# Performance work log

Measured on AMD Instinct MI355X. Metric: run time of the kernel, lower is better.

The kernel has to match this reference:

```python
import jax, jax.numpy as jnp
import numpy as np

NUM_NODES = 100000
NUM_EDGES = 1600000
EMBED_DIM = 128
NUM_CLASSES = 2
NUM_LAYERS = 3


def setup_inputs() -> dict:
    key = jax.random.key(0)
    k_row, k_col, k_val, k_emb, k_a, k_w, k_b = jax.random.split(key, 7)
    node_indices = jnp.arange(NUM_NODES, dtype=jnp.int64 if jax.config.read('jax_enable_x64') else jnp.int32)
    adj_row = jax.random.randint(k_row, (NUM_EDGES,), 0, NUM_NODES)
    adj_col = jax.random.randint(k_col, (NUM_EDGES,), 0, NUM_NODES)
    # symmetric-normalized-ish positive edge weights
    adj_val = jax.random.uniform(k_val, (NUM_EDGES,), dtype=jnp.float32) * (1.0 / 16.0)
    embedding = jax.random.normal(k_emb, (NUM_NODES, EMBED_DIM), dtype=jnp.float32)
    alpha = jnp.ones((NUM_LAYERS + 1,), dtype=jnp.float32) / (NUM_LAYERS + 1)
    W = jax.random.normal(k_w, (EMBED_DIM, NUM_CLASSES), dtype=jnp.float32) * 0.05
    b = jnp.zeros((NUM_CLASSES,), dtype=jnp.float32)
    return {
        'node_indices': node_indices, 'adj_row': adj_row, 'adj_col': adj_col,
        'adj_val': adj_val, 'embedding': embedding, 'alpha': alpha, 'W': W, 'b': b,
    }


def reference(node_indices, adj_row, adj_col, adj_val, embedding, alpha, W, b):
    # x: [N, D] embedding lookup
    x = embedding[node_indices]
    a = jax.nn.softmax(alpha)
    # alpha-weighted running sum over propagation layers (dropout in eval mode = identity)
    acc = a[0] * x
    cur = x
    for i in range(NUM_LAYERS):
        # sparse SpMM: out[r] += val * cur[c] for each edge (r, c)
        msgs = adj_val[:, None] * cur[adj_col]          # [E, D]
        cur = jax.ops.segment_sum(msgs, adj_row, num_segments=NUM_NODES)
        acc = acc + a[i + 1] * cur
    return acc @ W + b  # [N, num_classes]
```

## Files before the change

### kernel.cpp

```cpp
#include <hip/hip_runtime.h>

#define GD(x,y) (((x)+(y)-1)/(y))

#define SH    10
#define BPR   (1 << SH)
#define BS    256
#define KSPL  24
#define CAPSH 15
#define CAP   (1 << CAPSH)
#define CHUNK 2048

static __device__ __forceinline__ float2 ntload2(const float2* p){
    unsigned long long u = __builtin_nontemporal_load((const unsigned long long*)p);
    return *(float2*)&u;
}
static __device__ __forceinline__ void ntstore2(float2* p, float2 v){
    __builtin_nontemporal_store(*(unsigned long long*)&v, (unsigned long long*)p);
}

__global__ void init_k(int* __restrict__ cursor, int NBK,
                       const float* __restrict__ alpha, float* __restrict__ a, int na){
    int t = threadIdx.x;
    if (t < NBK) cursor[t] = t << CAPSH;
    if (t == 0){
        float m = alpha[0];
        for (int i = 1; i < na; ++i) m = fmaxf(m, alpha[i]);
        float s = 0.f;
        for (int i = 0; i < na; ++i){ float e = expf(alpha[i] - m); a[i] = e; s += e; }
        float inv = 1.f / s;
        for (int i = 0; i < na; ++i) a[i] *= inv;
    }
}

__global__ void fillproj_k(const int* __restrict__ row, const int* __restrict__ col,
                           const float* __restrict__ val, int* __restrict__ cursor,
                           int2* __restrict__ sep, int E, int NBK, int GF,
                           const float* __restrict__ emb, const int* __restrict__ idx,
                           const float* __restrict__ W, const float* __restrict__ bb,
                           const float* __restrict__ a, float* __restrict__ y,
                           float* __restrict__ out, int N){
    if (blockIdx.x < GF){
        __shared__ int2 staged[CHUNK];
        __shared__ unsigned char bid[CHUNK];
        __shared__ int h[128], sc[128], lstart[128], gbase[128], lcur[128];
        int t = threadIdx.x;
        int s = blockIdx.x * CHUNK;
        int e = min(E, s + CHUNK);
        int cnt = e - s;
        if (t < 128) h[t] = 0;
        __syncthreads();
        for (int base = s + t * 4; base < e; base += BS * 4){
            if (base + 3 < e){
                int4 r4 = *(const int4*)(row + base);
                atomicAdd(&h[r4.x >> SH], 1);
                atomicAdd(&h[r4.y >> SH], 1);
                atomicAdd(&h[r4.z >> SH], 1);
                atomicAdd(&h[r4.w >> SH], 1);
            } else {
                for (int j = 0; j < 4 && base + j < e; ++j)
                    atomicAdd(&h[row[base + j] >> SH], 1);
            }
        }
        __syncthreads();
        int v = (t < 128) ? h[t] : 0;
        if (t < 128) sc[t] = v;
        __syncthreads();
        #pragma unroll
        for (int off = 1; off < 128; off <<= 1){
            int add = (t < 128 && t >= off) ? sc[t - off] : 0;
            __syncthreads();
            if (t < 128) sc[t] += add;
            __syncthreads();
        }
        if (t < 128){
            int excl = sc[t] - v;
            lstart[t] = excl;
            lcur[t]   = excl;
            gbase[t]  = (v > 0) ? atomicAdd(&cursor[t], v) : 0;
        }
        __syncthreads();
        for (int base = s + t * 4; base < e; base += BS * 4){
            int r[4]; int c[4]; float vv[4];
            int m = min(4, e - base);
            if (m == 4){
                int4 r4 = *(const int4*)(row + base);
                int4 c4 = *(const int4*)(col + base);
                float4 v4 = *(const float4*)(val + base);
                r[0]=r4.x; r[1]=r4.y; r[2]=r4.z; r[3]=r4.w;
                c[0]=c4.x; c[1]=c4.y; c[2]=c4.z; c[3]=c4.w;
                vv[0]=v4.x; vv[1]=v4.y; vv[2]=v4.z; vv[3]=v4.w;
            } else {
                for (int j = 0; j < m; ++j){ r[j]=row[base+j]; c[j]=col[base+j]; vv[j]=val[base+j]; }
            }
            for (int j = 0; j < m; ++j){
                int b = r[j] >> SH;
                int lp = atomicAdd(&lcur[b], 1);
                int2 pk;
                pk.x = c[j] | ((r[j] & (BPR - 1)) << 17);
                pk.y = __float_as_int(vv[j]);
                staged[lp] = pk;
                bid[lp] = (unsigned char)b;
            }
        }
        __syncthreads();
        for (int i2 = t; i2 < cnt; i2 += BS){
            int b = bid[i2];
            sep[gbase[b] + (i2 - lstart[b])] = staged[i2];
        }
    } else {
        int gt = (blockIdx.x - GF) * BS + threadIdx.x;
        int w = gt >> 6;
        int lane = gt & 63;
        int n = w * 2 + (lane >> 5);
        if (n >= N) return;
        int sl = lane & 31;
        float4 x = ((const float4*)(emb + (size_t)idx[n] * 128))[sl];
        int d0 = 4 * sl;
        float s0 = x.x * W[d0*2]   + x.y * W[d0*2+2] + x.z * W[d0*2+4] + x.w * W[d0*2+6];
        float s1 = x.x * W[d0*2+1] + x.y * W[d0*2+3] + x.z * W[d0*2+5] + x.w * W[d0*2+7];
        #pragma unroll
        for (int off = 16; off; off >>= 1){
            s0 += __shfl_down(s0, off, 32);
            s1 += __shfl_down(s1, off, 32);
        }
        if (sl == 0){
            float c = a[0];
            ((float2*)y)[n]   = make_float2(s0, s1);
            ((float2*)out)[n] = make_float2(bb[0] + c * s0, bb[1] + c * s1);
        }
    }
}

__global__ void spmm_k(const int* __restrict__ cursor, const int2* __restrict__ sep,
                       const float* __restrict__ yin, float* __restrict__ partial,
                       int NBK){
    __shared__ float accx[BPR];
    __shared__ float accy[BPR];
    int b  = blockIdx.x / KSPL;
    int sp = blockIdx.x % KSPL;
    int t  = threadIdx.x;
    for (int j = t; j < BPR; j += BS){ accx[j] = 0.f; accy[j] = 0.f; }
    __syncthreads();
    int s = b << CAPSH;
    int e = cursor[b];
    int len = e - s, per = GD(len, KSPL);
    int cs = s + sp * per, ce = min(e, cs + per);
    int i = cs + t;
    for (; i + 3 * BS < ce; i += 4 * BS){
        int2 p0 = sep[i], p1 = sep[i + BS], p2 = sep[i + 2*BS], p3 = sep[i + 3*BS];
        float2 m0 = ((const float2*)yin)[p0.x & 0x1FFFF];
        float2 m1 = ((const float2*)yin)[p1.x & 0x1FFFF];
        float2 m2 = ((const float2*)yin)[p2.x & 0x1FFFF];
        float2 m3 = ((const float2*)yin)[p3.x & 0x1FFFF];
        float v0 = __int_as_float(p0.y), v1 = __int_as_float(p1.y);
        float v2 = __int_as_float(p2.y), v3 = __int_as_float(p3.y);
        atomicAdd(&accx[p0.x >> 17], v0 * m0.x); atomicAdd(&accy[p0.x >> 17], v0 * m0.y);
        atomicAdd(&accx[p1.x >> 17], v1 * m1.x); atomicAdd(&accy[p1.x >> 17], v1 * m1.y);
        atomicAdd(&accx[p2.x >> 17], v2 * m2.x); atomicAdd(&accy[p2.x >> 17], v2 * m2.y);
        atomicAdd(&accx[p3.x >> 17], v3 * m3.x); atomicAdd(&accy[p3.x >> 17], v3 * m3.y);
    }
    for (; i < ce; i += BS){
        int2 pk = sep[i];
        float v = __int_as_float(pk.y);
        float2 m = ((const float2*)yin)[pk.x & 0x1FFFF];
        atomicAdd(&accx[pk.x >> 17], v * m.x);
        atomicAdd(&accy[pk.x >> 17], v * m.y);
    }
    __syncthreads();
    float2* dst = (float2*)partial + (size_t)(b * KSPL + sp) * BPR;
    for (int j = t; j < BPR; j += BS)
        ntstore2(&dst[j], make_float2(accx[j], accy[j]));
}

__global__ void comb_k(const float* __restrict__ partial, const float* __restrict__ a,
                       int ai, float* __restrict__ ynext, float* __restrict__ out,
                       int N, int store){
    int n = blockIdx.x * blockDim.x + threadIdx.x;
    if (n >= N) return;
    int b = n >> SH, j = n & (BPR - 1);
    const float2* p = (const float2*)partial + (size_t)b * KSPL * BPR + j;
    float sx = 0.f, sy = 0.f;
    #pragma unroll
    for (int sp = 0; sp < KSPL; ++sp){
        float2 v = ntload2(&p[(size_t)sp * BPR]);
        sx += v.x; sy += v.y;
    }
    if (store) ((float2*)ynext)[n] = make_float2(sx, sy);
    float c = a[ai];
    float2 o = ((float2*)out)[n];
    o.x += c * sx; o.y += c * sy;
    ((float2*)out)[n] = o;
}

extern "C" void kernel_launch(void* const* d_in, const int* in_sizes, int n_in,
                              void* d_out, int out_size, void* d_ws, size_t ws_size,
                              hipStream_t stream) {
    const int*   node_idx = (const int*)  d_in[0];
    const int*   adj_row  = (const int*)  d_in[1];
    const int*   adj_col  = (const int*)  d_in[2];
    const float* adj_val  = (const float*)d_in[3];
    const float* emb      = (const float*)d_in[4];
    const float* alpha    = (const float*)d_in[5];
    const float* W        = (const float*)d_in[6];
    const float* b        = (const float*)d_in[7];
    float* out = (float*)d_out;

    const int N = in_sizes[0];
    const int E = in_sizes[1];
    const int L = in_sizes[5] - 1;
    const int NBK = GD(N, BPR);
    const int GF  = GD(E, CHUNK);
    const int GP  = GD(N * 32, BS);

    char* w = (char*)d_ws;
    float* yA     = (float*)w;  w += (size_t)N * 2 * 4;
    float* yB     = (float*)w;  w += (size_t)N * 2 * 4;
    float* partial= (float*)w;  w += (size_t)NBK * KSPL * BPR * 2 * 4;
    int2*  sep    = (int2*)w;   w += (size_t)NBK * CAP * 8;
    int*   cursor = (int*)w;    w += 1024;
    float* a      = (float*)w;

    init_k<<<1, 128, 0, stream>>>(cursor, NBK, alpha, a, L + 1);

    fillproj_k<<<GF + GP, BS, 0, stream>>>(adj_row, adj_col, adj_val, cursor, sep,
                                           E, NBK, GF, emb, node_idx, W, b, a,
                                           yA, out, N);

    float* ysrc = yA;
    float* ydst = yB;
    for (int i = 0; i < L; ++i){
        spmm_k<<<NBK * KSPL, BS, 0, stream>>>(cursor, sep, ysrc, partial, NBK);
        comb_k<<<GD(N, 256), 256, 0, stream>>>(partial, a, i + 1, ydst, out,
                                               N, (i < L - 1) ? 1 : 0);
        float* tmp = ysrc; ysrc = ydst; ydst = tmp;
    }
}
```

Baseline: 121.6 us.

## Shrink row bins to 128 rows and fuse SpMM combine into single-pass kernel

```diff
diff --git a/kernel.cpp b/kernel.cpp
--- a/kernel.cpp
+++ b/kernel.cpp
@@ -2,21 +2,12 @@
 
 #define GD(x,y) (((x)+(y)-1)/(y))
 
-#define SH    10
+#define SH    7
 #define BPR   (1 << SH)
 #define BS    256
-#define KSPL  24
-#define CAPSH 15
-#define CAP   (1 << CAPSH)
-#define CHUNK 2048
-
-static __device__ __forceinline__ float2 ntload2(const float2* p){
-    unsigned long long u = __builtin_nontemporal_load((const unsigned long long*)p);
-    return *(float2*)&u;
-}
-static __device__ __forceinline__ void ntstore2(float2* p, float2 v){
-    __builtin_nontemporal_store(*(unsigned long long*)&v, (unsigned long long*)p);
-}
+#define CAPSH 12
+#define CHUNK 4096
+#define MAXB  800
 
 __global__ void init_k(int* __restrict__ cursor, int NBK,
                        const float* __restrict__ alpha, float* __restrict__ a, int na){
@@ -41,44 +32,66 @@
                            float* __restrict__ out, int N){
     if (blockIdx.x < GF){
         __shared__ int2 staged[CHUNK];
-        __shared__ unsigned char bid[CHUNK];
-        __shared__ int h[128], sc[128], lstart[128], gbase[128], lcur[128];
+        __shared__ unsigned short bid[CHUNK];
+        __shared__ int h4[4 * MAXB];
+        __shared__ int lstart[MAXB];
+        __shared__ int gbase[MAXB];
+        __shared__ int sc[BS];
         int t = threadIdx.x;
+        int wv = t >> 6;
         int s = blockIdx.x * CHUNK;
         int e = min(E, s + CHUNK);
         int cnt = e - s;
-        if (t < 128) h[t] = 0;
-        __syncthreads();
+        for (int i = t; i < 4 * MAXB; i += BS) h4[i] = 0;
+        __syncthreads();
+        int* hw = h4 + wv * MAXB;
         for (int base = s + t * 4; base < e; base += BS * 4){
             if (base + 3 < e){
                 int4 r4 = *(const int4*)(row + base);
-                atomicAdd(&h[r4.x >> SH], 1);
-                atomicAdd(&h[r4.y >> SH], 1);
-                atomicAdd(&h[r4.z >> SH], 1);
-                atomicAdd(&h[r4.w >> SH], 1);
+                atomicAdd(&hw[r4.x >> SH], 1);
+                atomicAdd(&hw[r4.y >> SH], 1);
+                atomicAdd(&hw[r4.z >> SH], 1);
+                atomicAdd(&hw[r4.w >> SH], 1);
             } else {
                 for (int j = 0; j < 4 && base + j < e; ++j)
-                    atomicAdd(&h[row[base + j] >> SH], 1);
-            }
-        }
-        __syncthreads();
-        int v = (t < 128) ? h[t] : 0;
-        if (t < 128) sc[t] = v;
+                    atomicAdd(&hw[row[base + j] >> SH], 1);
+            }
+        }
+        __syncthreads();
+        int b0 = t * 4;
+        int tt0=0, tt1=0, tt2=0, tt3=0, tsum;
+        if (b0     < NBK) tt0 = h4[b0]     + h4[MAXB+b0]     + h4[2*MAXB+b0]     + h4[3*MAXB+b0];
+        if (b0 + 1 < NBK) tt1 = h4[b0+1]   + h4[MAXB+b0+1]   + h4[2*MAXB+b0+1]   + h4[3*MAXB+b0+1];
+        if (b0 + 2 < NBK) tt2 = h4[b0+2]   + h4[MAXB+b0+2]   + h4[2*MAXB+b0+2]   + h4[3*MAXB+b0+2];
+        if (b0 + 3 < NBK) tt3 = h4[b0+3]   + h4[MAXB+b0+3]   + h4[2*MAXB+b0+3]   + h4[3*MAXB+b0+3];
+        tsum = tt0 + tt1 + tt2 + tt3;
+        sc[t] = tsum;
         __syncthreads();
         #pragma unroll
-        for (int off = 1; off < 128; off <<= 1){
-            int add = (t < 128 && t >= off) ? sc[t - off] : 0;
+        for (int off = 1; off < BS; off <<= 1){
+            int add = (t >= off) ? sc[t - off] : 0;
             __syncthreads();
-            if (t < 128) sc[t] += add;
+            sc[t] += add;
             __syncthreads();
         }
-        if (t < 128){
-            int excl = sc[t] - v;
-            lstart[t] = excl;
-            lcur[t]   = excl;
-            gbase[t]  = (v > 0) ? atomicAdd(&cursor[t], v) : 0;
-        }
-        __syncthreads();
+        int run = sc[t] - tsum;
+        #pragma unroll
+        for (int j = 0; j < 4; ++j){
+            int bin = b0 + j;
+            int tj = (j == 0) ? tt0 : (j == 1) ? tt1 : (j == 2) ? tt2 : tt3;
+            if (bin < NBK){
+                int c0 = h4[bin], c1 = h4[MAXB+bin], c2 = h4[2*MAXB+bin];
+                lstart[bin] = run;
+                gbase[bin]  = (tj > 0) ? atomicAdd(&cursor[bin], tj) : 0;
+                h4[bin]          = run;
+                h4[MAXB+bin]     = run + c0;
+                h4[2*MAXB+bin]   = run + c0 + c1;
+                h4[3*MAXB+bin]   = run + c0 + c1 + c2;
+                run += tj;
+            }
+        }
+        __syncthreads();
+        int* lcw = h4 + wv * MAXB;
         for (int base = s + t * 4; base < e; base += BS * 4){
             int r[4]; int c[4]; float vv[4];
             int m = min(4, e - base);
@@ -94,12 +107,12 @@
             }
             for (int j = 0; j < m; ++j){
                 int b = r[j] >> SH;
-                int lp = atomicAdd(&lcur[b], 1);
+                int lp = atomicAdd(&lcw[b], 1);
                 int2 pk;
                 pk.x = c[j] | ((r[j] & (BPR - 1)) << 17);
                 pk.y = __float_as_int(vv[j]);
                 staged[lp] = pk;
-                bid[lp] = (unsigned char)b;
+                bid[lp] = (unsigned short)b;
             }
         }
         __syncthreads();
@@ -132,21 +145,19 @@
 }
 
 __global__ void spmm_k(const int* __restrict__ cursor, const int2* __restrict__ sep,
-                       const float* __restrict__ yin, float* __restrict__ partial,
-                       int NBK){
+                       const float* __restrict__ yin, float* __restrict__ ynext,
+                       const float* __restrict__ a, int ai, float* __restrict__ out,
+                       int N, int store){
     __shared__ float accx[BPR];
     __shared__ float accy[BPR];
-    int b  = blockIdx.x / KSPL;
-    int sp = blockIdx.x % KSPL;
+    int sb = blockIdx.x;
     int t  = threadIdx.x;
-    for (int j = t; j < BPR; j += BS){ accx[j] = 0.f; accy[j] = 0.f; }
+    if (t < BPR){ accx[t] = 0.f; accy[t] = 0.f; }
     __syncthreads();
-    int s = b << CAPSH;
-    int e = cursor[b];
-    int len = e - s, per = GD(len, KSPL);
-    int cs = s + sp * per, ce = min(e, cs + per);
-    int i = cs + t;
-    for (; i + 3 * BS < ce; i += 4 * BS){
+    int s = sb << CAPSH;
+    int e = cursor[sb];
+    int i = s + t;
+    for (; i + 3 * BS < e; i += 4 * BS){
         int2 p0 = sep[i], p1 = sep[i + BS], p2 = sep[i + 2*BS], p3 = sep[i + 3*BS];
         float2 m0 = ((const float2*)yin)[p0.x & 0x1FFFF];
         float2 m1 = ((const float2*)yin)[p1.x & 0x1FFFF];
@@ -159,7 +170,7 @@
         atomicAdd(&accx[p2.x >> 17], v2 * m2.x); atomicAdd(&accy[p2.x >> 17], v2 * m2.y);
         atomicAdd(&accx[p3.x >> 17], v3 * m3.x); atomicAdd(&accy[p3.x >> 17], v3 * m3.y);
     }
-    for (; i < ce; i += BS){
+    for (; i < e; i += BS){
         int2 pk = sep[i];
         float v = __int_as_float(pk.y);
         float2 m = ((const float2*)yin)[pk.x & 0x1FFFF];
@@ -167,29 +178,17 @@
         atomicAdd(&accy[pk.x >> 17], v * m.y);
     }
     __syncthreads();
-    float2* dst = (float2*)partial + (size_t)(b * KSPL + sp) * BPR;
-    for (int j = t; j < BPR; j += BS)
-        ntstore2(&dst[j], make_float2(accx[j], accy[j]));
-}
-
-__global__ void comb_k(const float* __restrict__ partial, const float* __restrict__ a,
-                       int ai, float* __restrict__ ynext, float* __restrict__ out,
-                       int N, int store){
-    int n = blockIdx.x * blockDim.x + threadIdx.x;
-    if (n >= N) return;
-    int b = n >> SH, j = n & (BPR - 1);
-    const float2* p = (const float2*)partial + (size_t)b * KSPL * BPR + j;
-    float sx = 0.f, sy = 0.f;
-    #pragma unroll
-    for (int sp = 0; sp < KSPL; ++sp){
-        float2 v = ntload2(&p[(size_t)sp * BPR]);
-        sx += v.x; sy += v.y;
-    }
-    if (store) ((float2*)ynext)[n] = make_float2(sx, sy);
-    float c = a[ai];
-    float2 o = ((float2*)out)[n];
-    o.x += c * sx; o.y += c * sy;
-    ((float2*)out)[n] = o;
+    if (t < BPR){
+        int n = (sb << SH) + t;
+        if (n < N){
+            float2 z = make_float2(accx[t], accy[t]);
+            if (store) ((float2*)ynext)[n] = z;
+            float c = a[ai];
+            float2 o = ((float2*)out)[n];
+            o.x += c * z.x; o.y += c * z.y;
+            ((float2*)out)[n] = o;
+        }
+    }
 }
 
 extern "C" void kernel_launch(void* const* d_in, const int* in_sizes, int n_in,
@@ -215,12 +214,11 @@
     char* w = (char*)d_ws;
     float* yA     = (float*)w;  w += (size_t)N * 2 * 4;
     float* yB     = (float*)w;  w += (size_t)N * 2 * 4;
-    float* partial= (float*)w;  w += (size_t)NBK * KSPL * BPR * 2 * 4;
-    int2*  sep    = (int2*)w;   w += (size_t)NBK * CAP * 8;
-    int*   cursor = (int*)w;    w += 1024;
+    int2*  sep    = (int2*)w;   w += ((size_t)NBK << CAPSH) * 8;
+    int*   cursor = (int*)w;    w += (size_t)MAXB * 4 + 1024;
     float* a      = (float*)w;
 
-    init_k<<<1, 128, 0, stream>>>(cursor, NBK, alpha, a, L + 1);
+    init_k<<<1, 1024, 0, stream>>>(cursor, NBK, alpha, a, L + 1);
 
     fillproj_k<<<GF + GP, BS, 0, stream>>>(adj_row, adj_col, adj_val, cursor, sep,
                                            E, NBK, GF, emb, node_idx, W, b, a,
@@ -229,9 +227,8 @@
     float* ysrc = yA;
     float* ydst = yB;
     for (int i = 0; i < L; ++i){
-        spmm_k<<<NBK * KSPL, BS, 0, stream>>>(cursor, sep, ysrc, partial, NBK);
-        comb_k<<<GD(N, 256), 256, 0, stream>>>(partial, a, i + 1, ydst, out,
-                                               N, (i < L - 1) ? 1 : 0);
+        spmm_k<<<NBK, BS, 0, stream>>>(cursor, sep, ysrc, ydst, a, i + 1,
+                                       out, N, (i < L - 1) ? 1 : 0);
         float* tmp = ysrc; ysrc = ydst; ydst = tmp;
     }
 }
```

Result: slower. 148.8 us (+22.3%).
